# Kernel tuning notes

Measured on AMD Instinct MI355X. Metric: run time of the kernel, lower is better.

## Reference

```python
import jax, jax.numpy as jnp
import numpy as np


def setup_inputs() -> dict:
    key = jax.random.key(0)
    k1, k2 = jax.random.split(key)
    H = W = 2048
    valid = jnp.ones((H, W), dtype=bool)  # all pixels valid (index_map >= 0)
    candidates = jax.random.normal(k1, (H * W, 3), dtype=jnp.float32)
    candidates_norms = jax.random.normal(k2, (H * W, 3), dtype=jnp.float32)
    return {"valid": valid, "candidates": candidates,
            "candidates_norms": candidates_norms, "step": 2}


def _graph_outputs(valid, candidates, candidates_norms, step):
    # Grid-mesh graph build (init_graph) with all-valid map, expressed with
    # static shapes: invalid (out-of-grid) edges/faces are masked, not pruned.
    H, W = valid.shape
    us = jnp.arange(0, W - 1, step)
    vs = jnp.arange(0, H - 1, step)
    nu, nv = us.shape[0], vs.shape[0]
    N = nu * nv  # number of ED nodes (anchors)
    jj, ii = jnp.meshgrid(jnp.arange(nv), jnp.arange(nu), indexing='ij')
    jj = jj.ravel(); ii = ii.ravel()
    node = jj * nu + ii                      # node id == arange(N)
    pix = vs[jj] * W + us[ii]                # flattened pixel index of anchor
    pts = candidates[pix]                    # [N,3] ED node positions
    nrm = candidates_norms[pix]              # [N,3] ED node normals

    re = ii + 1 < nu                         # right neighbor exists
    de = jj + 1 < nv                         # down neighbor exists
    rd = re & de
    # 4-edge stencil per anchor: right, diag, down, anti-diag (matches init_graph)
    src = jnp.concatenate([node, node, node, node + 1])
    dst = jnp.concatenate([node + 1, node + nu + 1, node + nu, node + nu])
    emask = jnp.concatenate([re, rd, de, rd])          # [4N]
    srcs = jnp.where(emask, src, 0)
    dsts = jnp.where(emask, dst, 0)
    diff = pts[srcs] - pts[dsts]
    sq = jnp.sum(diff * diff, axis=1)
    w = emask.astype(pts.dtype)
    lens = jnp.sqrt(jnp.where(emask, sq, 1.0)) * w     # masked edge lengths

    # radii[k] = mean length of edges incident to node k (scatter-mean replaces
    # the original O(N) Python loop over torch.any(edge_index == k))
    ssum = (jax.ops.segment_sum(lens, srcs, num_segments=N)
            + jax.ops.segment_sum(lens, dsts, num_segments=N))
    cnt = (jax.ops.segment_sum(w, srcs, num_segments=N)
           + jax.ops.segment_sum(w, dsts, num_segments=N))
    radii = ssum / jnp.maximum(cnt, 1.0)
    has = cnt > 0
    mean_r = jnp.sum(jnp.where(has, radii, 0.0)) / jnp.maximum(
        jnp.sum(has.astype(pts.dtype)), 1.0)
    radii = jnp.where(has, radii, mean_r)  # NaN fix: fill isolated nodes w/ mean

    # two triangles per grid cell: (a, right, diag) and (a, diag, down)
    t0 = jnp.concatenate([node, node])
    t1 = jnp.concatenate([node + 1, node + nu + 1])
    t2 = jnp.concatenate([node + nu + 1, node + nu])
    tmask = jnp.concatenate([rd, rd])
    t0s = jnp.where(tmask, t0, 0)
    t1s = jnp.where(tmask, t1, 0)
    t2s = jnp.where(tmask, t2, 0)
    cr = jnp.cross(pts[t1s] - pts[t0s], pts[t2s] - pts[t0s], axis=1)
    areas = 0.5 * jnp.sqrt(jnp.sum(cr * cr, axis=1) + 1e-13)
    areas = areas * tmask.astype(pts.dtype)
    return pts, nrm, radii, lens, areas


def reference(valid, candidates, candidates_norms, step):
    return _graph_outputs(valid, candidates, candidates_norms, step)
```

## Files before the change

kernel.cpp:

```cpp
#include <hip/hip_runtime.h>
#include <math.h>


struct F3 { float x, y, z; };

__device__ inline F3 ldp(const float* __restrict__ p, long o) {
    F3 r; r.x = p[o]; r.y = p[o + 1]; r.z = p[o + 2]; return r;
}

__device__ inline float dist3(const F3& a, const F3& b) {
    float dx = a.x - b.x, dy = a.y - b.y, dz = a.z - b.z;
    return sqrtf(dx * dx + dy * dy + dz * dz);
}

__global__ __launch_bounds__(256) void ddg_kernel(
    const float* __restrict__ cand, const float* __restrict__ cnorm,
    float* __restrict__ out, int W, int nu, int nv, int step)
{
    const int n = blockIdx.x * 256 + threadIdx.x;
    const int N = nu * nv;
    if (n >= N) return;
    const int ii = n % nu;
    const int jj = n / nu;
    const bool hr = (ii + 1) < nu;
    const bool hd = (jj + 1) < nv;
    const bool hl = ii > 0;
    const bool hu = jj > 0;

    const long dR = (long)step * 3;
    const long dD = (long)step * W * 3;
    const long base = (long)(jj * step) * W * 3 + (long)(ii * step) * 3;

    const F3 z{0.f, 0.f, 0.f};
    const F3 p00 = ldp(cand, base);
    const F3 n00 = ldp(cnorm, base);
    const F3 pr  = hr         ? ldp(cand, base + dR)      : z;
    const F3 pd  = hd         ? ldp(cand, base + dD)      : z;
    const F3 prd = (hr && hd) ? ldp(cand, base + dR + dD) : z;
    const F3 pld = (hl && hd) ? ldp(cand, base - dR + dD) : z;
    const F3 pl  = hl         ? ldp(cand, base - dR)      : z;
    const F3 plu = (hl && hu) ? ldp(cand, base - dR - dD) : z;
    const F3 pu  = hu         ? ldp(cand, base - dD)      : z;
    const F3 pru = (hr && hu) ? ldp(cand, base + dR - dD) : z;

    const float len_r  = hr         ? dist3(p00, pr)  : 0.f;
    const float len_dg = (hr && hd) ? dist3(p00, prd) : 0.f;
    const float len_dn = hd         ? dist3(p00, pd)  : 0.f;
    const float len_ad = (hr && hd) ? dist3(pr, pd)   : 0.f;

    float a0 = 0.f, a1 = 0.f;
    if (hr && hd) {
        const float e1x = pr.x - p00.x,  e1y = pr.y - p00.y,  e1z = pr.z - p00.z;
        const float e2x = prd.x - p00.x, e2y = prd.y - p00.y, e2z = prd.z - p00.z;
        const float cx = e1y * e2z - e1z * e2y;
        const float cy = e1z * e2x - e1x * e2z;
        const float cz = e1x * e2y - e1y * e2x;
        a0 = 0.5f * sqrtf(cx * cx + cy * cy + cz * cz + 1e-13f);
        const float f2x = pd.x - p00.x, f2y = pd.y - p00.y, f2z = pd.z - p00.z;
        const float gx = e2y * f2z - e2z * f2y;
        const float gy = e2z * f2x - e2x * f2z;
        const float gz = e2x * f2y - e2y * f2x;
        a1 = 0.5f * sqrtf(gx * gx + gy * gy + gz * gz + 1e-13f);
    }

    float s = 0.f, cnt = 0.f;
    if (hr)       { s += len_r;           cnt += 1.f; }
    if (hr && hd) { s += len_dg;          cnt += 1.f; }
    if (hd)       { s += len_dn;          cnt += 1.f; }
    if (hl && hd) { s += dist3(p00, pld); cnt += 1.f; }
    if (hl)       { s += dist3(p00, pl);  cnt += 1.f; }
    if (hl && hu) { s += dist3(p00, plu); cnt += 1.f; }
    if (hu)       { s += dist3(p00, pu);  cnt += 1.f; }
    if (hr && hu) { s += dist3(p00, pru); cnt += 1.f; }
    const float radius = s / fmaxf(cnt, 1.f);

    float* __restrict__ pts   = out;
    float* __restrict__ nrm   = out + 3L * N;
    float* __restrict__ rad   = out + 6L * N;
    float* __restrict__ lens  = out + 7L * N;
    float* __restrict__ areas = out + 11L * N;

    pts[3L * n]     = p00.x; pts[3L * n + 1] = p00.y; pts[3L * n + 2] = p00.z;
    nrm[3L * n]     = n00.x; nrm[3L * n + 1] = n00.y; nrm[3L * n + 2] = n00.z;
    rad[n]          = radius;
    lens[n]             = len_r;
    lens[(long)N + n]   = len_dg;
    lens[2L * N + n]    = len_dn;
    lens[3L * N + n]    = len_ad;
    areas[n]            = a0;
    areas[(long)N + n]  = a1;
}

extern "C" void kernel_launch(void* const* d_in, const int* in_sizes, int n_in,
                              void* d_out, int out_size, void* d_ws, size_t ws_size,
                              hipStream_t stream) {
    const float* cand  = (const float*)d_in[1];
    const float* cnorm = (const float*)d_in[2];
    const int step = 2;
    const int HW = in_sizes[0];
    const int W = (int)(sqrt((double)HW) + 0.5);
    const int nu = (W - 1 + step - 1) / step;
    const int nv = nu;
    const int N = nu * nv;
    const int blocks = (N + 255) / 256;
    ddg_kernel<<<blocks, 256, 0, stream>>>(cand, cnorm, (float*)d_out, W, nu, nv, step);
}
```

Measured before the change: 147.1 us.

## Stage stencil rows in shared memory via 2D tiles with float4 loads

Replaces the 1D per-node launch with 64x4 2D tiles that cooperatively load the six candidate rows and four normal rows they need into LDS using aligned float4 global loads. Each node then reads its nine neighbours from shared memory instead of issuing strided scalar global loads. This targets redundant and uncoalesced global traffic, since each anchor row was previously fetched up to three times by different nodes. In exchange it adds a __syncthreads, about 16KB of LDS per block, and index arithmetic for halo and boundary clamping. Only even pixel rows are ever used, so roughly half of each loaded row is discarded.

```diff
diff --git a/kernel.cpp b/kernel.cpp
--- a/kernel.cpp
+++ b/kernel.cpp
@@ -2,9 +2,16 @@
 #include <math.h>
 
 
+#define BX 64
+#define BY 4
+#define NC 131
+#define RS (NC * 3)
+#define RSP 400
+#define NF4 100
+
 struct F3 { float x, y, z; };
 
-__device__ inline F3 ldp(const float* __restrict__ p, long o) {
+__device__ inline F3 ldl(const float* p, int o) {
     F3 r; r.x = p[o]; r.y = p[o + 1]; r.z = p[o + 2]; return r;
 }
 
@@ -15,52 +22,86 @@
 
 __global__ __launch_bounds__(256) void ddg_kernel(
     const float* __restrict__ cand, const float* __restrict__ cnorm,
-    float* __restrict__ out, int W, int nu, int nv, int step)
+    float* __restrict__ out, int W, int nu, int nv)
 {
-    const int n = blockIdx.x * 256 + threadIdx.x;
+    __shared__ float sC[6 * RSP];
+    __shared__ float sN[4 * RSP];
+
+    const int H = W;
+    const int tx = threadIdx.x, ty = threadIdx.y;
+    const int tid = ty * BX + tx;
+    const int i0 = blockIdx.x * BX;
+    const int j0 = blockIdx.y * BY;
+    const long c0 = 2L * i0 - 2;
+
+    const float4* __restrict__ cand4  = (const float4*)cand;
+    const float4* __restrict__ cnorm4 = (const float4*)cnorm;
+
+    for (int idx = tid; idx < 10 * NF4; idx += BX * BY) {
+        const int k = idx / NF4;
+        const int t = idx - k * NF4;
+        const bool isC = k < 6;
+        int r = isC ? (2 * j0 - 2 + 2 * k) : (2 * (j0 + (k - 6)));
+        r = min(max(r, 0), H - 2);
+        const long f0 = ((long)r * W + c0) * 3;
+        const long a0 = (f0 < 0 ? 0L : f0) & ~3L;
+        const long q  = (a0 >> 2) + t;
+        const float4 v = isC ? cand4[q] : cnorm4[q];
+        const long G = q << 2;
+        const long l = G - f0;
+        float* dst = isC ? (sC + k * RSP) : (sN + (k - 6) * RSP);
+        const float vv[4] = {v.x, v.y, v.z, v.w};
+        #pragma unroll
+        for (int c = 0; c < 4; ++c) {
+            const long lc = l + c;
+            if (lc >= 0 && lc < RS) dst[lc] = vv[c];
+        }
+    }
+    __syncthreads();
+
+    const int ii = i0 + tx, jj = j0 + ty;
+    if (ii >= nu || jj >= nv) return;
     const int N = nu * nv;
-    if (n >= N) return;
-    const int ii = n % nu;
-    const int jj = n / nu;
-    const bool hr = (ii + 1) < nu;
-    const bool hd = (jj + 1) < nv;
-    const bool hl = ii > 0;
-    const bool hu = jj > 0;
+    const int n = jj * nu + ii;
+    const bool hr = (ii + 1) < nu, hd = (jj + 1) < nv;
+    const bool hl = ii > 0,        hu = jj > 0;
 
-    const long dR = (long)step * 3;
-    const long dD = (long)step * W * 3;
-    const long base = (long)(jj * step) * W * 3 + (long)(ii * step) * 3;
+    const float* rU = sC + ty * RSP;
+    const float* rM = sC + (ty + 1) * RSP;
+    const float* rD = sC + (ty + 2) * RSP;
+    const int lL = (2 * tx) * 3;
+    const int lM = (2 * tx + 2) * 3;
+    const int lR = (2 * tx + 4) * 3;
 
-    const F3 z{0.f, 0.f, 0.f};
-    const F3 p00 = ldp(cand, base);
-    const F3 n00 = ldp(cnorm, base);
-    const F3 pr  = hr         ? ldp(cand, base + dR)      : z;
-    const F3 pd  = hd         ? ldp(cand, base + dD)      : z;
-    const F3 prd = (hr && hd) ? ldp(cand, base + dR + dD) : z;
-    const F3 pld = (hl && hd) ? ldp(cand, base - dR + dD) : z;
-    const F3 pl  = hl         ? ldp(cand, base - dR)      : z;
-    const F3 plu = (hl && hu) ? ldp(cand, base - dR - dD) : z;
-    const F3 pu  = hu         ? ldp(cand, base - dD)      : z;
-    const F3 pru = (hr && hu) ? ldp(cand, base + dR - dD) : z;
+    const F3 p00 = ldl(rM, lM);
+    const F3 pr  = ldl(rM, lR);
+    const F3 pl  = ldl(rM, lL);
+    const F3 pu  = ldl(rU, lM);
+    const F3 pd  = ldl(rD, lM);
+    const F3 prd = ldl(rD, lR);
+    const F3 pld = ldl(rD, lL);
+    const F3 plu = ldl(rU, lL);
+    const F3 pru = ldl(rU, lR);
+    const F3 n00 = ldl(sN + ty * RSP, lM);
 
     const float len_r  = hr         ? dist3(p00, pr)  : 0.f;
     const float len_dg = (hr && hd) ? dist3(p00, prd) : 0.f;
     const float len_dn = hd         ? dist3(p00, pd)  : 0.f;
     const float len_ad = (hr && hd) ? dist3(pr, pd)   : 0.f;
 
-    float a0 = 0.f, a1 = 0.f;
+    float a0f = 0.f, a1f = 0.f;
     if (hr && hd) {
         const float e1x = pr.x - p00.x,  e1y = pr.y - p00.y,  e1z = pr.z - p00.z;
         const float e2x = prd.x - p00.x, e2y = prd.y - p00.y, e2z = prd.z - p00.z;
         const float cx = e1y * e2z - e1z * e2y;
         const float cy = e1z * e2x - e1x * e2z;
         const float cz = e1x * e2y - e1y * e2x;
-        a0 = 0.5f * sqrtf(cx * cx + cy * cy + cz * cz + 1e-13f);
+        a0f = 0.5f * sqrtf(cx * cx + cy * cy + cz * cz + 1e-13f);
         const float f2x = pd.x - p00.x, f2y = pd.y - p00.y, f2z = pd.z - p00.z;
         const float gx = e2y * f2z - e2z * f2y;
         const float gy = e2z * f2x - e2x * f2z;
         const float gz = e2x * f2y - e2y * f2x;
-        a1 = 0.5f * sqrtf(gx * gx + gy * gy + gz * gz + 1e-13f);
+        a1f = 0.5f * sqrtf(gx * gx + gy * gy + gz * gz + 1e-13f);
     }
 
     float s = 0.f, cnt = 0.f;
@@ -87,8 +128,8 @@
     lens[(long)N + n]   = len_dg;
     lens[2L * N + n]    = len_dn;
     lens[3L * N + n]    = len_ad;
-    areas[n]            = a0;
-    areas[(long)N + n]  = a1;
+    areas[n]            = a0f;
+    areas[(long)N + n]  = a1f;
 }
 
 extern "C" void kernel_launch(void* const* d_in, const int* in_sizes, int n_in,
@@ -101,7 +142,7 @@
     const int W = (int)(sqrt((double)HW) + 0.5);
     const int nu = (W - 1 + step - 1) / step;
     const int nv = nu;
-    const int N = nu * nv;
-    const int blocks = (N + 255) / 256;
-    ddg_kernel<<<blocks, 256, 0, stream>>>(cand, cnorm, (float*)d_out, W, nu, nv, step);
+    dim3 block(BX, BY);
+    dim3 grid((nu + BX - 1) / BX, (nv + BY - 1) / BY);
+    ddg_kernel<<<grid, block, 0, stream>>>(cand, cnorm, (float*)d_out, W, nu, nv);
 }
```

Result: no change. 146.7 us (-0.3%).
